# Optimization experiments

Measured on AMD Instinct MI355X. Metric: run time of the kernel, lower is better.

The kernel has to match this reference:

```python
import jax, jax.numpy as jnp
import numpy as np

FRACS = (0.25, 0.5, 0.25)  # per-expert top-fraction kept, from the original forward


def setup_inputs() -> dict:
    key = jax.random.key(0)
    ks = jax.random.split(key, 10)
    B, S, D, P, E, C = 1, 65536, 1024, 512, 3, 2
    s = 0.02
    return {
        "hidden_states": jax.random.normal(ks[0], (B, S, D), jnp.float32),
        "W_t1": jax.random.normal(ks[1], (D, P), jnp.float32) * s,   # TransMIL stand-in proj
        "W_cls1": jax.random.normal(ks[2], (P, C), jnp.float32) * s, # trans1 bag classifier
        "Wg0": jax.random.normal(ks[3], (P, 2), jnp.float32) * s,    # gate
        "Wg1": jax.random.normal(ks[4], (P, 2), jnp.float32) * s,    # gate1
        "Wg2": jax.random.normal(ks[5], (P, 2), jnp.float32) * s,    # gate2
        "W_clf": jax.random.normal(ks[6], (E, P, E), jnp.float32) * s,  # per-expert classifiers
        "W_a1": jax.random.normal(ks[7], (P, P), jnp.float32) * s,   # agg1 TransMIL stand-in proj
        "W_acls": jax.random.normal(ks[8], (P, C), jnp.float32) * s, # agg1 bag classifier
    }


def reference(hidden_states, W_t1, W_cls1, Wg0, Wg1, Wg2, W_clf, W_a1, W_acls):
    B, S, D = hidden_states.shape
    x = hidden_states.reshape(-1, D)               # (T, D) tokens
    T = x.shape[0]
    # trans1 (TransMIL stand-in): per-patch feature + mean-pool bag logits
    patches = jnp.tanh(x @ W_t1)                   # (T, P) patch_feature
    bag = patches.mean(0)
    Y_logits = (bag @ W_cls1)[None, :]             # (1, C)
    Y_prob = jax.nn.softmax(Y_logits, -1)
    Y_hat = jnp.argmax(Y_logits, -1)
    # three independent routers, softmax + top-1
    router_logits = patches @ Wg0                  # (T, 2)
    rw0 = jax.nn.softmax(router_logits.astype(jnp.float32), -1)
    w_top0 = rw0.max(-1)                           # top-1 routing weight (gate0) used as sort key for ALL experts
    sel0 = jnp.argmax(rw0, -1)
    sel1 = jnp.argmax(jax.nn.softmax((patches @ Wg1).astype(jnp.float32), -1), -1)
    sel2 = jnp.argmax(jax.nn.softmax((patches @ Wg2).astype(jnp.float32), -1), -1)
    masks = [sel0 == 1, sel1 == 1, sel2 == 1]      # expert_mask[e][1] token selection
    joint_losses = jnp.float32(0.0)
    sel_fs, nums_list = [], []
    for e in range(3):
        mask = masks[e]
        cnt = mask.sum().astype(jnp.int32)
        nums = jnp.floor(cnt.astype(jnp.float32) * FRACS[e]).astype(jnp.int32)
        nums = jnp.where(nums == 0, cnt, nums)     # 'if nums != 0 else all' branch
        key_ = jnp.where(mask, w_top0, -jnp.inf)
        order = jnp.argsort(-key_)                 # descending routing weight
        rank = jnp.zeros(T, jnp.int32).at[order].set(jnp.arange(T, dtype=jnp.int32))
        sel = mask & (rank < nums)                 # top-fraction tokens of this expert
        sel_f = sel.astype(patches.dtype)
        mean_feat = (patches * sel_f[:, None]).sum(0) / jnp.maximum(nums, 1).astype(patches.dtype)
        logits = mean_feat @ W_clf[e]              # (3,)
        if e < 2:                                  # CE loss only for experts 0,1
            joint_losses = joint_losses + (-jax.nn.log_softmax(logits)[e])
        sel_fs.append(sel_f)
        nums_list.append(nums)
    # agg1 (TransMIL stand-in) over concatenated represent_patchs == multiplicity-weighted mean
    feats2 = jnp.tanh(patches @ W_a1)              # (T, P)
    total_sel = sel_fs[0] + sel_fs[1] + sel_fs[2]
    total_n = (nums_list[0] + nums_list[1] + nums_list[2]).astype(patches.dtype)
    agg_bag = (feats2 * total_sel[:, None]).sum(0) / jnp.maximum(total_n, 1.0)
    e_Y_logits = (agg_bag @ W_acls)[None, :]
    e_Y_hat = jnp.argmax(e_Y_logits, -1)
    distribute = jnp.stack([jnp.asarray(T, jnp.int32), nums_list[0], nums_list[1], nums_list[2]])
    return (e_Y_logits, e_Y_hat, Y_logits, Y_prob, Y_hat, router_logits, joint_losses, distribute)
```

## Files before the change

### kernel.cpp

```cpp
#include <hip/hip_runtime.h>
#include <cstdint>
#include <cstddef>

#define T_TOK 65536
#define DDIM  1024
#define PDIM  512

typedef __attribute__((ext_vector_type(8))) short          shortx8;
typedef __attribute__((ext_vector_type(8))) unsigned short ushortx8;
typedef __attribute__((ext_vector_type(4))) float          floatx4;

__device__ __forceinline__ unsigned short f2bf_rn(float x){
  unsigned int u = __float_as_uint(x);
  unsigned int r = u + 0x7FFFu + ((u >> 16) & 1u);
  return (unsigned short)(r >> 16);
}
__device__ __forceinline__ float bf2f(unsigned short h){
  return __uint_as_float(((unsigned int)h) << 16);
}
__device__ __forceinline__ float ftanh(float x){
  float ez = __expf(2.f * x);
  return 1.f - 2.f / (ez + 1.f);
}

__global__ void prep(const float* __restrict__ Wt1, const float* __restrict__ Wa1,
                     unsigned short* __restrict__ W1th, unsigned short* __restrict__ W1tl,
                     unsigned short* __restrict__ Wath, unsigned short* __restrict__ Watl,
                     int* __restrict__ zbase)
{
  int gid = blockIdx.x * 256 + threadIdx.x;
  if (gid < 20544){ zbase[gid] = 0; return; }
  int i = gid - 20544;
  if (i < 524288){
    int p = i >> 10, k = i & 1023;
    float x = Wt1[(size_t)k * PDIM + p];
    unsigned short h = f2bf_rn(x);
    W1th[i] = h;
    W1tl[i] = f2bf_rn(x - bf2f(h));
    return;
  }
  i -= 524288;
  if (i < 262144){
    int n = i >> 9, k = i & 511;
    float x = Wa1[(size_t)k * PDIM + n];
    unsigned short h = f2bf_rn(x);
    Wath[i] = h;
    Watl[i] = f2bf_rn(x - bf2f(h));
  }
}

template<int MODE>
__global__ __launch_bounds__(256, 2)
void gemm_split(const float* __restrict__ A,
                const unsigned short* __restrict__ Bhg,
                const unsigned short* __restrict__ Blg,
                float* __restrict__ Cout,
                float* __restrict__ colacc,
                const int* __restrict__ cidx,
                const float* __restrict__ wgt,
                const int* __restrict__ params)
{
  constexpr int K = (MODE == 0) ? 1024 : 512;
  __shared__ unsigned short Ah[128][40];
  __shared__ unsigned short Al[128][40];
  __shared__ unsigned short Bh[128][40];
  __shared__ unsigned short Bl[128][40];
  __shared__ int   cidxl[128];
  __shared__ float wl[128];

  const int tid = threadIdx.x;
  const int m0 = blockIdx.y * 128;
  const int n0 = blockIdx.x * 128;

  if (MODE == 1){
    int count = params[21];
    if (m0 >= count) return;
    if (tid < 128){
      int g = m0 + tid;
      if (g < count){ cidxl[tid] = cidx[g]; wl[tid] = wgt[g]; }
      else          { cidxl[tid] = 0;       wl[tid] = 0.f;   }
    }
    __syncthreads();
  }

  const int lane = tid & 63;
  const int wv   = tid >> 6;
  const int wm   = (wv & 1) << 6;
  const int wn   = (wv >> 1) << 6;
  const int lr   = lane & 15;
  const int quad = lane >> 4;
  const int kb8  = quad << 3;

  floatx4 acc[4][4];
  #pragma unroll
  for (int i = 0; i < 4; i++)
    #pragma unroll
    for (int j = 0; j < 4; j++)
      acc[i][j] = (floatx4){0.f, 0.f, 0.f, 0.f};

  const int nkb = K >> 5;
  for (int kb = 0; kb < nkb; ++kb){
    const int k0 = kb << 5;
    #pragma unroll
    for (int i = 0; i < 4; i++){
      int lin = i * 256 + tid;
      int row = lin >> 3;
      int kq  = (lin & 7) << 2;
      size_t arow = (MODE == 0) ? (size_t)(m0 + row) : (size_t)cidxl[row];
      const float4 v = *(const float4*)(A + arow * K + k0 + kq);
      unsigned int ux = __float_as_uint(v.x), uy = __float_as_uint(v.y);
      unsigned int uz = __float_as_uint(v.z), uw = __float_as_uint(v.w);
      float rx = v.x - __uint_as_float(ux & 0xFFFF0000u);
      float ry = v.y - __uint_as_float(uy & 0xFFFF0000u);
      float rz = v.z - __uint_as_float(uz & 0xFFFF0000u);
      float rw = v.w - __uint_as_float(uw & 0xFFFF0000u);
      ushort4 h, l;
      h.x = (unsigned short)(ux >> 16); l.x = (unsigned short)(__float_as_uint(rx) >> 16);
      h.y = (unsigned short)(uy >> 16); l.y = (unsigned short)(__float_as_uint(ry) >> 16);
      h.z = (unsigned short)(uz >> 16); l.z = (unsigned short)(__float_as_uint(rz) >> 16);
      h.w = (unsigned short)(uw >> 16); l.w = (unsigned short)(__float_as_uint(rw) >> 16);
      *(ushort4*)&Ah[row][kq] = h;
      *(ushort4*)&Al[row][kq] = l;
    }
    #pragma unroll
    for (int i = 0; i < 2; i++){
      int lin = i * 256 + tid;
      int row = lin >> 2;
      int kq  = (lin & 3) << 3;
      size_t off = (size_t)(n0 + row) * K + k0 + kq;
      *(ushortx8*)&Bh[row][kq] = *(const ushortx8*)(Bhg + off);
      *(ushortx8*)&Bl[row][kq] = *(const ushortx8*)(Blg + off);
    }
    __syncthreads();
    shortx8 a0[4], a1[4], b0[4], b1[4];
    #pragma unroll
    for (int i = 0; i < 4; i++){
      a0[i] = *(const shortx8*)&Ah[wm + i * 16 + lr][kb8];
      a1[i] = *(const shortx8*)&Al[wm + i * 16 + lr][kb8];
      b0[i] = *(const shortx8*)&Bh[wn + i * 16 + lr][kb8];
      b1[i] = *(const shortx8*)&Bl[wn + i * 16 + lr][kb8];
    }
    #pragma unroll
    for (int i = 0; i < 4; i++){
      #pragma unroll
      for (int j = 0; j < 4; j++){
        acc[i][j] = __builtin_amdgcn_mfma_f32_16x16x32_bf16(a0[i], b0[j], acc[i][j], 0, 0, 0);
        acc[i][j] = __builtin_amdgcn_mfma_f32_16x16x32_bf16(a1[i], b0[j], acc[i][j], 0, 0, 0);
        acc[i][j] = __builtin_amdgcn_mfma_f32_16x16x32_bf16(a0[i], b1[j], acc[i][j], 0, 0, 0);
      }
    }
    __syncthreads();
  }

  float csum[4] = {0.f, 0.f, 0.f, 0.f};
  #pragma unroll
  for (int i = 0; i < 4; i++){
    float w0 = 1.f, w1 = 1.f, w2 = 1.f, w3 = 1.f;
    if (MODE == 1){
      const float4 wv4 = *(const float4*)&wl[wm + i * 16 + (quad << 2)];
      w0 = wv4.x; w1 = wv4.y; w2 = wv4.z; w3 = wv4.w;
    }
    #pragma unroll
    for (int j = 0; j < 4; j++){
      float t0 = ftanh(acc[i][j][0]);
      float t1 = ftanh(acc[i][j][1]);
      float t2 = ftanh(acc[i][j][2]);
      float t3 = ftanh(acc[i][j][3]);
      if (MODE == 0){
        size_t base = (size_t)(m0 + wm + i * 16 + (quad << 2)) * PDIM + (n0 + wn + j * 16 + lr);
        Cout[base]            = t0;
        Cout[base +     PDIM] = t1;
        Cout[base + 2 * PDIM] = t2;
        Cout[base + 3 * PDIM] = t3;
        csum[j] += t0 + t1 + t2 + t3;
      } else {
        csum[j] += t0 * w0 + t1 * w1 + t2 * w2 + t3 * w3;
      }
    }
  }
  #pragma unroll
  for (int j = 0; j < 4; j++){
    float s = csum[j];
    s += __shfl_xor(s, 16);
    s += __shfl_xor(s, 32);
    if (lane < 16) atomicAdd(&colacc[n0 + wn + j * 16 + lane], s);
  }
}

__global__ void gates_kernel(const float* __restrict__ patches,
                             const float* __restrict__ Wg0,
                             const float* __restrict__ Wg1,
                             const float* __restrict__ Wg2,
                             float* __restrict__ dout,
                             unsigned int* __restrict__ wkey,
                             unsigned char* __restrict__ mask3,
                             int* __restrict__ params,
                             int* __restrict__ hist)
{
  __shared__ int lc[3];
  const int tid = threadIdx.x;
  if (tid < 3) lc[tid] = 0;
  __syncthreads();
  const int lane = tid & 63;
  float wg[3][16];
  const float* Wgp[3] = {Wg0, Wg1, Wg2};
  #pragma unroll
  for (int g = 0; g < 3; g++){
    #pragma unroll
    for (int j = 0; j < 4; j++){
      float4 v = *(const float4*)(Wgp[g] + lane * 16 + j * 4);
      wg[g][j * 4 + 0] = v.x; wg[g][j * 4 + 1] = v.y;
      wg[g][j * 4 + 2] = v.z; wg[g][j * 4 + 3] = v.w;
    }
  }
  const int nw = gridDim.x << 2;
  for (int t = blockIdx.x * 4 + (tid >> 6); t < T_TOK; t += nw){
    const float* row = patches + (size_t)t * PDIM + lane * 8;
    float4 v0 = *(const float4*)row;
    float4 v1 = *(const float4*)(row + 4);
    float x[8] = {v0.x, v0.y, v0.z, v0.w, v1.x, v1.y, v1.z, v1.w};
    float g00 = 0, g01 = 0, g10 = 0, g11 = 0, g20 = 0, g21 = 0;
    #pragma unroll
    for (int j = 0; j < 8; j++){
      g00 += x[j] * wg[0][2 * j]; g01 += x[j] * wg[0][2 * j + 1];
      g10 += x[j] * wg[1][2 * j]; g11 += x[j] * wg[1][2 * j + 1];
      g20 += x[j] * wg[2][2 * j]; g21 += x[j] * wg[2][2 * j + 1];
    }
    #pragma unroll
    for (int off = 1; off < 64; off <<= 1){
      g00 += __shfl_xor(g00, off); g01 += __shfl_xor(g01, off);
      g10 += __shfl_xor(g10, off); g11 += __shfl_xor(g11, off);
      g20 += __shfl_xor(g20, off); g21 += __shfl_xor(g21, off);
    }
    if (lane == 0){
      dout[8 + 2 * t]     = g00;
      dout[8 + 2 * t + 1] = g01;
      int m0 = g01 > g00;
      int m1 = g11 > g10;
      int m2 = g21 > g20;
      mask3[t] = (unsigned char)(m0 | (m1 << 1) | (m2 << 2));
      float d = fabsf(g00 - g01);
      float w = 1.0f / (1.0f + __expf(-d));
      unsigned int u = __float_as_uint(w);
      u = u < 0x3F000000u ? 0x3F000000u : u;
      u = u > 0x3F7FFFFFu ? 0x3F7FFFFFu : u;
      wkey[t] = u;
      int b = (int)((u >> 11) & 0xFFFu);
      if (m0){ atomicAdd(&hist[b], 1);         atomicAdd(&lc[0], 1); }
      if (m1){ atomicAdd(&hist[4096 + b], 1);  atomicAdd(&lc[1], 1); }
      if (m2){ atomicAdd(&hist[8192 + b], 1);  atomicAdd(&lc[2], 1); }
    }
  }
  __syncthreads();
  if (tid < 3 && lc[tid]) atomicAdd(&params[tid], lc[tid]);
}

__global__ void find_bucket(int* __restrict__ params, const int* __restrict__ hist)
{
  __shared__ int cs[256], orig[256];
  __shared__ int selc, selrk;
  const int tid = threadIdx.x;
  for (int e = 0; e < 3; e++){
    int cnt = params[e];
    int shift = (e == 1) ? 1 : 2;
    int nums = cnt >> shift;
    if (nums == 0) nums = cnt;
    if (tid == 0) params[3 + e] = nums;
    __syncthreads();
    if (nums == 0){
      if (tid == 0){ params[6 + e] = -1; params[9 + e] = 0; }
      __syncthreads();
      continue;
    }
    const int* h = hist + e * 4096 + tid * 16;
    int s = 0;
    #pragma unroll
    for (int j = 0; j < 16; j++) s += h[j];
    cs[tid] = s; orig[tid] = s;
    __syncthreads();
    for (int off = 1; off < 256; off <<= 1){
      int v = (tid + off < 256) ? cs[tid + off] : 0;
      __syncthreads();
      cs[tid] += v;
      __syncthreads();
    }
    if (cs[tid] >= nums && (cs[tid] - orig[tid]) < nums){
      selc = tid; selrk = nums - (cs[tid] - orig[tid]);
    }
    __syncthreads();
    if (tid == 0){
      int ch = selc, rk = selrk;
      const int* hh = hist + e * 4096 + ch * 16;
      int acc = 0;
      for (int j = 15; j >= 0; j--){
        int c = hh[j];
        if (acc + c >= rk){ params[6 + e] = ch * 16 + j; params[9 + e] = rk - acc; break; }
        acc += c;
      }
    }
    __syncthreads();
  }
}

__global__ void level2hist(const int* __restrict__ params, const unsigned int* __restrict__ wkey,
                           const unsigned char* __restrict__ mask3, int* __restrict__ h2)
{
  const int e = blockIdx.y;
  const int B = params[6 + e];
  if (B < 0) return;
  const unsigned char bit = (unsigned char)(1u << e);
  const int t0 = blockIdx.x * 2048 + threadIdx.x;
  #pragma unroll
  for (int i = 0; i < 8; i++){
    int t = t0 + i * 256;
    if (mask3[t] & bit){
      unsigned int u = wkey[t];
      if ((int)((u >> 11) & 0xFFFu) == B) atomicAdd(&h2[e * 2048 + (u & 2047u)], 1);
    }
  }
}

__global__ void find_theta(int* __restrict__ params, const int* __restrict__ h2)
{
  const int e = blockIdx.x;
  const int tid = threadIdx.x;
  __shared__ int cs[256], orig[256];
  __shared__ int selc;
  int B = params[6 + e], rank = params[9 + e];
  if (B < 0){
    if (tid == 0){ params[12 + e] = (int)0xFFFFFFFFu; params[15 + e] = 0; params[18 + e] = 0; }
    return;
  }
  const int* h = h2 + e * 2048 + tid * 8;
  int s = 0;
  #pragma unroll
  for (int j = 0; j < 8; j++) s += h[j];
  cs[tid] = s; orig[tid] = s;
  __syncthreads();
  for (int off = 1; off < 256; off <<= 1){
    int v = (tid + off < 256) ? cs[tid + off] : 0;
    __syncthreads();
    cs[tid] += v;
    __syncthreads();
  }
  if (cs[tid] >= rank && (cs[tid] - orig[tid]) < rank) selc = tid;
  __syncthreads();
  if (tid == 0){
    int ch = selc;
    int rk = rank - (cs[ch] - orig[ch]);
    const int* hh = h2 + e * 2048 + ch * 8;
    int acc = 0;
    for (int j = 7; j >= 0; j--){
      int c = hh[j];
      if (acc + c >= rk){
        int sub = ch * 8 + j;
        params[12 + e] = (int)(0x3F000000u | ((unsigned)B << 11) | (unsigned)sub);
        params[15 + e] = rk - acc;
        params[18 + e] = c;
        break;
      }
      acc += c;
    }
  }
}

__global__ void mark_sel(const int* __restrict__ params, const unsigned int* __restrict__ wkey,
                         const unsigned char* __restrict__ mask3, unsigned char* __restrict__ selb)
{
  const int e = blockIdx.y;
  const int bx = blockIdx.x;
  const int tid = threadIdx.x;
  const unsigned int theta = (unsigned int)params[12 + e];
  const int r = params[15 + e];
  const int ceq = params[18 + e];
  const unsigned char bit = (unsigned char)(1u << e);
  unsigned char* sb = selb + e * T_TOK;
  if (ceq == r){
    int t0 = bx * 2048;
    #pragma unroll
    for (int i = 0; i < 8; i++){
      int t = t0 + i * 256 + tid;
      unsigned char mk = mask3[t] & bit;
      sb[t] = (mk && wkey[t] >= theta) ? 1 : 0;
    }
  } else {
    if (bx) return;
    __shared__ int basec;
    __shared__ int wsum[4];
    if (tid == 0) basec = 0;
    __syncthreads();
    const int lane = tid & 63, w = tid >> 6;
    for (int c = 0; c < 256; c++){
      int t = c * 256 + tid;
      unsigned char mk = mask3[t] & bit;
      unsigned int u = mk ? wkey[t] : 0u;
      bool gt = mk && (u > theta);
      bool eq = mk && (u == theta);
      unsigned long long bal = __ballot(eq);
      if (lane == 0) wsum[w] = __popcll(bal);
      __syncthreads();
      int wbase = 0;
      for (int ww = 0; ww < w; ww++) wbase += wsum[ww];
      int pos = basec + wbase + __popcll(bal & ((1ull << lane) - 1ull));
      sb[t] = (gt || (eq && pos < r)) ? 1 : 0;
      __syncthreads();
      if (tid == 0) basec += wsum[0] + wsum[1] + wsum[2] + wsum[3];
      __syncthreads();
    }
  }
}

__global__ void compact(const unsigned char* __restrict__ selb, int* __restrict__ cidx,
                        float* __restrict__ wgt, int* __restrict__ params)
{
  int t = blockIdx.x * 256 + threadIdx.x;
  int ts = selb[t] + selb[T_TOK + t] + selb[2 * T_TOK + t];
  int lane = threadIdx.x & 63;
  unsigned long long bal = __ballot(ts > 0);
  int base = 0;
  if (lane == 0) base = atomicAdd(&params[21], __popcll(bal));
  base = __shfl(base, 0);
  if (ts){
    int pos = base + __popcll(bal & ((1ull << lane) - 1ull));
    cidx[pos] = t;
    wgt[pos] = (float)ts;
  }
}

__global__ void meanfeat_c(const float* __restrict__ patches, const unsigned char* __restrict__ selb,
                           const int* __restrict__ cidx, const int* __restrict__ params,
                           float* __restrict__ mf)
{
  const int count = params[21];
  const int base = blockIdx.x * 256;
  if (base >= count) return;
  const int n = min(256, count - base);
  const int tid = threadIdx.x;
  __shared__ int cl[256];
  __shared__ unsigned char f0s[256], f1s[256];
  if (tid < n){
    int c = cidx[base + tid];
    cl[tid] = c;
    f0s[tid] = selb[c];
    f1s[tid] = selb[T_TOK + c];
  }
  __syncthreads();
  float s00 = 0, s01 = 0, s10 = 0, s11 = 0;
  for (int i = 0; i < n; i++){
    int f0 = f0s[i], f1 = f1s[i];
    if (f0 | f1){
      float2 v = *(const float2*)(patches + (size_t)cl[i] * PDIM + tid * 2);
      if (f0){ s00 += v.x; s01 += v.y; }
      if (f1){ s10 += v.x; s11 += v.y; }
    }
  }
  atomicAdd(&mf[tid * 2],       s00);
  atomicAdd(&mf[tid * 2 + 1],   s01);
  atomicAdd(&mf[512 + tid * 2],     s10);
  atomicAdd(&mf[512 + tid * 2 + 1], s11);
}

__global__ void finalize(const float* __restrict__ bagsum, const float* __restrict__ aggsum,
                         const float* __restrict__ mf, const int* __restrict__ params,
                         const float* __restrict__ Wcls1, const float* __restrict__ Wclf,
                         const float* __restrict__ Wacls, float* __restrict__ dout)
{
  const int lane = threadIdx.x;
  const int nums0 = params[3], nums1 = params[4], nums2 = params[5];
  const float invT = 1.0f / 65536.0f;
  const float inv0 = 1.0f / (float)(nums0 > 0 ? nums0 : 1);
  const float inv1 = 1.0f / (float)(nums1 > 0 ? nums1 : 1);
  const float totn = (float)(nums0 + nums1 + nums2);
  const float invA = 1.0f / fmaxf(totn, 1.0f);
  float y0 = 0, y1 = 0, a0 = 0, a1 = 0;
  float l00 = 0, l01 = 0, l02 = 0, l10 = 0, l11 = 0, l12 = 0;
  #pragma unroll
  for (int j = 0; j < 8; j++){
    int p = lane * 8 + j;
    float bg = bagsum[p] * invT;
    y0 += bg * Wcls1[p * 2]; y1 += bg * Wcls1[p * 2 + 1];
    float ag = aggsum[p] * invA;
    a0 += ag * Wacls[p * 2]; a1 += ag * Wacls[p * 2 + 1];
    float m0v = mf[p] * inv0;
    l00 += m0v * Wclf[p * 3]; l01 += m0v * Wclf[p * 3 + 1]; l02 += m0v * Wclf[p * 3 + 2];
    float m1v = mf[512 + p] * inv1;
    l10 += m1v * Wclf[1536 + p * 3]; l11 += m1v * Wclf[1536 + p * 3 + 1]; l12 += m1v * Wclf[1536 + p * 3 + 2];
  }
  #pragma unroll
  for (int off = 1; off < 64; off <<= 1){
    y0 += __shfl_xor(y0, off);   y1 += __shfl_xor(y1, off);
    a0 += __shfl_xor(a0, off);   a1 += __shfl_xor(a1, off);
    l00 += __shfl_xor(l00, off); l01 += __shfl_xor(l01, off); l02 += __shfl_xor(l02, off);
    l10 += __shfl_xor(l10, off); l11 += __shfl_xor(l11, off); l12 += __shfl_xor(l12, off);
  }
  if (lane == 0){
    dout[0] = a0; dout[1] = a1;
    dout[2] = (a1 > a0) ? 1.0f : 0.0f;
    dout[3] = y0; dout[4] = y1;
    float mx = fmaxf(y0, y1), e0 = expf(y0 - mx), e1 = expf(y1 - mx), inv = 1.0f / (e0 + e1);
    dout[5] = e0 * inv; dout[6] = e1 * inv;
    dout[7] = (y1 > y0) ? 1.0f : 0.0f;
    float m3 = fmaxf(fmaxf(l00, l01), l02);
    float lse0 = m3 + logf(expf(l00 - m3) + expf(l01 - m3) + expf(l02 - m3));
    float m4 = fmaxf(fmaxf(l10, l11), l12);
    float lse1 = m4 + logf(expf(l10 - m4) + expf(l11 - m4) + expf(l12 - m4));
    dout[131080] = (lse0 - l00) + (lse1 - l11);
    dout[131081] = 65536.0f;
    dout[131082] = (float)nums0;
    dout[131083] = (float)nums1;
    dout[131084] = (float)nums2;
  }
}

extern "C" void kernel_launch(void* const* d_in, const int* in_sizes, int n_in,
                              void* d_out, int out_size, void* d_ws, size_t ws_size,
                              hipStream_t stream)
{
  const float* X      = (const float*)d_in[0];
  const float* W_t1   = (const float*)d_in[1];
  const float* W_cls1 = (const float*)d_in[2];
  const float* Wg0    = (const float*)d_in[3];
  const float* Wg1    = (const float*)d_in[4];
  const float* Wg2    = (const float*)d_in[5];
  const float* W_clf  = (const float*)d_in[6];
  const float* W_a1   = (const float*)d_in[7];
  const float* W_acls = (const float*)d_in[8];
  float* dout = (float*)d_out;
  char* ws = (char*)d_ws;

  float*          patches = (float*)         (ws + 0);
  unsigned short* W1th    = (unsigned short*)(ws + 134217728);
  unsigned short* W1tl    = (unsigned short*)(ws + 135266304);
  unsigned short* Wath    = (unsigned short*)(ws + 136314880);
  unsigned short* Watl    = (unsigned short*)(ws + 136839168);
  unsigned int*   wkey    = (unsigned int*)  (ws + 137363456);
  unsigned char*  mask3   = (unsigned char*) (ws + 137625600);
  unsigned char*  selb    = (unsigned char*) (ws + 137691136);
  int*            cidx    = (int*)           (ws + 137887744);
  float*          wgt     = (float*)         (ws + 138149888);
  int*            zbase   = (int*)           (ws + 138412032);
  int*            hist    = zbase;
  int*            h2      = zbase + 12288;
  int*            params  = zbase + 18432;
  float*          bagsum  = (float*)(zbase + 18496);
  float*          aggsum  = (float*)(zbase + 19008);
  float*          mf      = (float*)(zbase + 19520);

  prep<<<3153, 256, 0, stream>>>(W_t1, W_a1, W1th, W1tl, Wath, Watl, zbase);

  gemm_split<0><<<dim3(4, 512), 256, 0, stream>>>(
      X, W1th, W1tl, patches, bagsum, nullptr, nullptr, nullptr);

  gates_kernel<<<512, 256, 0, stream>>>(
      patches, Wg0, Wg1, Wg2, dout, wkey, mask3, params, hist);

  find_bucket<<<1, 256, 0, stream>>>(params, hist);
  level2hist<<<dim3(32, 3), 256, 0, stream>>>(params, wkey, mask3, h2);
  find_theta<<<3, 256, 0, stream>>>(params, h2);
  mark_sel<<<dim3(32, 3), 256, 0, stream>>>(params, wkey, mask3, selb);
  compact<<<256, 256, 0, stream>>>(selb, cidx, wgt, params);

  meanfeat_c<<<256, 256, 0, stream>>>(patches, selb, cidx, params, mf);

  gemm_split<1><<<dim3(4, 512), 256, 0, stream>>>(
      patches, Wath, Watl, nullptr, aggsum, cidx, wgt, params);

  finalize<<<1, 64, 0, stream>>>(bagsum, aggsum, mf, params, W_cls1, W_clf, W_acls, dout);
}
```

Baseline: 716.8 us.

## Fuse gate logits into main GEMM, store patches as bf16, swizzle LDS

The router-gate dot products now run in the epilogue of the first GEMM. Partial logits are reduced with shuffles and atomically added into a per-token buffer, so the separate pass that re-read the full fp32 patches matrix is gone. Patches are stored as bf16, which halves that write and the later reads. The second GEMM drops the split-precision low parts and runs a single bf16 MFMA. LDS tiles use an XOR swizzle instead of padding, and occupancy rises to 4 blocks per SM; the cost is lower precision in the router logits and the downstream aggregation, plus many more atomics.

```diff
diff --git a/kernel.cpp b/kernel.cpp
--- a/kernel.cpp
+++ b/kernel.cpp
@@ -22,15 +22,28 @@
   float ez = __expf(2.f * x);
   return 1.f - 2.f / (ez + 1.f);
 }
+__device__ __forceinline__ int lds_off(int row, int q){
+  return row * 32 + ((q ^ ((row >> 1) & 3)) << 3);
+}
+__device__ __forceinline__ void split8(const float4& a, const float4& b,
+                                       ushortx8& h, ushortx8& l){
+  float x[8] = {a.x, a.y, a.z, a.w, b.x, b.y, b.z, b.w};
+  #pragma unroll
+  for (int i = 0; i < 8; i++){
+    unsigned int u = __float_as_uint(x[i]);
+    float r = x[i] - __uint_as_float(u & 0xFFFF0000u);
+    h[i] = (unsigned short)(u >> 16);
+    l[i] = (unsigned short)(__float_as_uint(r) >> 16);
+  }
+}
 
 __global__ void prep(const float* __restrict__ Wt1, const float* __restrict__ Wa1,
                      unsigned short* __restrict__ W1th, unsigned short* __restrict__ W1tl,
-                     unsigned short* __restrict__ Wath, unsigned short* __restrict__ Watl,
-                     int* __restrict__ zbase)
+                     unsigned short* __restrict__ Wath, int* __restrict__ zbase)
 {
   int gid = blockIdx.x * 256 + threadIdx.x;
-  if (gid < 20544){ zbase[gid] = 0; return; }
-  int i = gid - 20544;
+  if (gid < 413760){ zbase[gid] = 0; return; }
+  int i = gid - 413760;
   if (i < 524288){
     int p = i >> 10, k = i & 1023;
     float x = Wt1[(size_t)k * PDIM + p];
@@ -42,46 +55,29 @@
   i -= 524288;
   if (i < 262144){
     int n = i >> 9, k = i & 511;
-    float x = Wa1[(size_t)k * PDIM + n];
-    unsigned short h = f2bf_rn(x);
-    Wath[i] = h;
-    Watl[i] = f2bf_rn(x - bf2f(h));
-  }
-}
-
-template<int MODE>
-__global__ __launch_bounds__(256, 2)
-void gemm_split(const float* __restrict__ A,
-                const unsigned short* __restrict__ Bhg,
-                const unsigned short* __restrict__ Blg,
-                float* __restrict__ Cout,
-                float* __restrict__ colacc,
-                const int* __restrict__ cidx,
-                const float* __restrict__ wgt,
-                const int* __restrict__ params)
-{
-  constexpr int K = (MODE == 0) ? 1024 : 512;
-  __shared__ unsigned short Ah[128][40];
-  __shared__ unsigned short Al[128][40];
-  __shared__ unsigned short Bh[128][40];
-  __shared__ unsigned short Bl[128][40];
-  __shared__ int   cidxl[128];
-  __shared__ float wl[128];
+    Wath[i] = f2bf_rn(Wa1[(size_t)k * PDIM + n]);
+  }
+}
+
+__global__ __launch_bounds__(256, 4)
+void gemm_main(const float* __restrict__ A,
+               const unsigned short* __restrict__ Bhg,
+               const unsigned short* __restrict__ Blg,
+               unsigned short* __restrict__ Ptch,
+               float* __restrict__ bagsum,
+               float* __restrict__ glog,
+               const float* __restrict__ Wg0,
+               const float* __restrict__ Wg1,
+               const float* __restrict__ Wg2)
+{
+  __shared__ __align__(16) unsigned short Ah[4096];
+  __shared__ __align__(16) unsigned short Al[4096];
+  __shared__ __align__(16) unsigned short Bh[4096];
+  __shared__ __align__(16) unsigned short Bl[4096];
 
   const int tid = threadIdx.x;
   const int m0 = blockIdx.y * 128;
   const int n0 = blockIdx.x * 128;
-
-  if (MODE == 1){
-    int count = params[21];
-    if (m0 >= count) return;
-    if (tid < 128){
-      int g = m0 + tid;
-      if (g < count){ cidxl[tid] = cidx[g]; wl[tid] = wgt[g]; }
-      else          { cidxl[tid] = 0;       wl[tid] = 0.f;   }
-    }
-    __syncthreads();
-  }
 
   const int lane = tid & 63;
   const int wv   = tid >> 6;
@@ -89,7 +85,11 @@
   const int wn   = (wv >> 1) << 6;
   const int lr   = lane & 15;
   const int quad = lane >> 4;
-  const int kb8  = quad << 3;
+
+  const int arow = tid >> 1;
+  const int akh  = (tid & 1) << 4;
+  const int aq0  = (tid & 1) << 1;
+  const float* asrc = A + (size_t)(m0 + arow) * DDIM + akh;
 
   floatx4 acc[4][4];
   #pragma unroll
@@ -98,47 +98,41 @@
     for (int j = 0; j < 4; j++)
       acc[i][j] = (floatx4){0.f, 0.f, 0.f, 0.f};
 
-  const int nkb = K >> 5;
-  for (int kb = 0; kb < nkb; ++kb){
+  for (int kb = 0; kb < 32; ++kb){
     const int k0 = kb << 5;
+    {
+      float4 v0 = *(const float4*)(asrc + k0);
+      float4 v1 = *(const float4*)(asrc + k0 + 4);
+      float4 v2 = *(const float4*)(asrc + k0 + 8);
+      float4 v3 = *(const float4*)(asrc + k0 + 12);
+      ushortx8 h0, l0, h1, l1;
+      split8(v0, v1, h0, l0);
+      split8(v2, v3, h1, l1);
+      *(ushortx8*)&Ah[lds_off(arow, aq0)]     = h0;
+      *(ushortx8*)&Ah[lds_off(arow, aq0 + 1)] = h1;
+      *(ushortx8*)&Al[lds_off(arow, aq0)]     = l0;
+      *(ushortx8*)&Al[lds_off(arow, aq0 + 1)] = l1;
+    }
+    #pragma unroll
+    for (int it = 0; it < 2; it++){
+      int lin = it * 256 + tid;
+      int row = lin >> 2;
+      int qb  = lin & 3;
+      size_t off = (size_t)(n0 + row) * DDIM + k0 + qb * 8;
+      ushortx8 bh = *(const ushortx8*)(Bhg + off);
+      ushortx8 bl = *(const ushortx8*)(Blg + off);
+      int d = lds_off(row, qb);
+      *(ushortx8*)&Bh[d] = bh;
+      *(ushortx8*)&Bl[d] = bl;
+    }
+    __syncthreads();
+    shortx8 a0[4], a1[4], b0[4], b1[4];
     #pragma unroll
     for (int i = 0; i < 4; i++){
-      int lin = i * 256 + tid;
-      int row = lin >> 3;
-      int kq  = (lin & 7) << 2;
-      size_t arow = (MODE == 0) ? (size_t)(m0 + row) : (size_t)cidxl[row];
-      const float4 v = *(const float4*)(A + arow * K + k0 + kq);
-      unsigned int ux = __float_as_uint(v.x), uy = __float_as_uint(v.y);
-      unsigned int uz = __float_as_uint(v.z), uw = __float_as_uint(v.w);
-      float rx = v.x - __uint_as_float(ux & 0xFFFF0000u);
-      float ry = v.y - __uint_as_float(uy & 0xFFFF0000u);
-      float rz = v.z - __uint_as_float(uz & 0xFFFF0000u);
-      float rw = v.w - __uint_as_float(uw & 0xFFFF0000u);
-      ushort4 h, l;
-      h.x = (unsigned short)(ux >> 16); l.x = (unsigned short)(__float_as_uint(rx) >> 16);
-      h.y = (unsigned short)(uy >> 16); l.y = (unsigned short)(__float_as_uint(ry) >> 16);
-      h.z = (unsigned short)(uz >> 16); l.z = (unsigned short)(__float_as_uint(rz) >> 16);
-      h.w = (unsigned short)(uw >> 16); l.w = (unsigned short)(__float_as_uint(rw) >> 16);
-      *(ushort4*)&Ah[row][kq] = h;
-      *(ushort4*)&Al[row][kq] = l;
-    }
-    #pragma unroll
-    for (int i = 0; i < 2; i++){
-      int lin = i * 256 + tid;
-      int row = lin >> 2;
-      int kq  = (lin & 3) << 3;
-      size_t off = (size_t)(n0 + row) * K + k0 + kq;
-      *(ushortx8*)&Bh[row][kq] = *(const ushortx8*)(Bhg + off);
-      *(ushortx8*)&Bl[row][kq] = *(const ushortx8*)(Blg + off);
-    }
-    __syncthreads();
-    shortx8 a0[4], a1[4], b0[4], b1[4];
-    #pragma unroll
-    for (int i = 0; i < 4; i++){
-      a0[i] = *(const shortx8*)&Ah[wm + i * 16 + lr][kb8];
-      a1[i] = *(const shortx8*)&Al[wm + i * 16 + lr][kb8];
-      b0[i] = *(const shortx8*)&Bh[wn + i * 16 + lr][kb8];
-      b1[i] = *(const shortx8*)&Bl[wn + i * 16 + lr][kb8];
+      a0[i] = *(const shortx8*)&Ah[lds_off(wm + i * 16 + lr, quad)];
+      a1[i] = *(const shortx8*)&Al[lds_off(wm + i * 16 + lr, quad)];
+      b0[i] = *(const shortx8*)&Bh[lds_off(wn + i * 16 + lr, quad)];
+      b1[i] = *(const shortx8*)&Bl[lds_off(wn + i * 16 + lr, quad)];
     }
     #pragma unroll
     for (int i = 0; i < 4; i++){
@@ -152,30 +146,58 @@
     __syncthreads();
   }
 
+  float wgr[4][6];
+  #pragma unroll
+  for (int j = 0; j < 4; j++){
+    int c = n0 + wn + j * 16 + lr;
+    wgr[j][0] = Wg0[c * 2]; wgr[j][1] = Wg0[c * 2 + 1];
+    wgr[j][2] = Wg1[c * 2]; wgr[j][3] = Wg1[c * 2 + 1];
+    wgr[j][4] = Wg2[c * 2]; wgr[j][5] = Wg2[c * 2 + 1];
+  }
+
   float csum[4] = {0.f, 0.f, 0.f, 0.f};
   #pragma unroll
   for (int i = 0; i < 4; i++){
-    float w0 = 1.f, w1 = 1.f, w2 = 1.f, w3 = 1.f;
-    if (MODE == 1){
-      const float4 wv4 = *(const float4*)&wl[wm + i * 16 + (quad << 2)];
-      w0 = wv4.x; w1 = wv4.y; w2 = wv4.z; w3 = wv4.w;
-    }
+    float gp[4][6];
+    #pragma unroll
+    for (int k = 0; k < 4; k++)
+      #pragma unroll
+      for (int g = 0; g < 6; g++) gp[k][g] = 0.f;
+    const int row = m0 + wm + i * 16 + quad * 4;
     #pragma unroll
     for (int j = 0; j < 4; j++){
       float t0 = ftanh(acc[i][j][0]);
       float t1 = ftanh(acc[i][j][1]);
       float t2 = ftanh(acc[i][j][2]);
       float t3 = ftanh(acc[i][j][3]);
-      if (MODE == 0){
-        size_t base = (size_t)(m0 + wm + i * 16 + (quad << 2)) * PDIM + (n0 + wn + j * 16 + lr);
-        Cout[base]            = t0;
-        Cout[base +     PDIM] = t1;
-        Cout[base + 2 * PDIM] = t2;
-        Cout[base + 3 * PDIM] = t3;
-        csum[j] += t0 + t1 + t2 + t3;
-      } else {
-        csum[j] += t0 * w0 + t1 * w1 + t2 * w2 + t3 * w3;
+      const int col = n0 + wn + j * 16 + lr;
+      Ptch[(size_t)(row + 0) * PDIM + col] = f2bf_rn(t0);
+      Ptch[(size_t)(row + 1) * PDIM + col] = f2bf_rn(t1);
+      Ptch[(size_t)(row + 2) * PDIM + col] = f2bf_rn(t2);
+      Ptch[(size_t)(row + 3) * PDIM + col] = f2bf_rn(t3);
+      csum[j] += t0 + t1 + t2 + t3;
+      #pragma unroll
+      for (int g = 0; g < 6; g++){
+        gp[0][g] += t0 * wgr[j][g];
+        gp[1][g] += t1 * wgr[j][g];
+        gp[2][g] += t2 * wgr[j][g];
+        gp[3][g] += t3 * wgr[j][g];
       }
+    }
+    #pragma unroll
+    for (int s = 1; s < 16; s <<= 1){
+      #pragma unroll
+      for (int k = 0; k < 4; k++)
+        #pragma unroll
+        for (int g = 0; g < 6; g++)
+          gp[k][g] += __shfl_xor(gp[k][g], s);
+    }
+    if (lr == 0){
+      #pragma unroll
+      for (int k = 0; k < 4; k++)
+        #pragma unroll
+        for (int g = 0; g < 6; g++)
+          atomicAdd(&glog[(size_t)(row + k) * 6 + g], gp[k][g]);
     }
   }
   #pragma unroll
@@ -183,74 +205,38 @@
     float s = csum[j];
     s += __shfl_xor(s, 16);
     s += __shfl_xor(s, 32);
-    if (lane < 16) atomicAdd(&colacc[n0 + wn + j * 16 + lane], s);
-  }
-}
-
-__global__ void gates_kernel(const float* __restrict__ patches,
-                             const float* __restrict__ Wg0,
-                             const float* __restrict__ Wg1,
-                             const float* __restrict__ Wg2,
-                             float* __restrict__ dout,
-                             unsigned int* __restrict__ wkey,
-                             unsigned char* __restrict__ mask3,
-                             int* __restrict__ params,
-                             int* __restrict__ hist)
+    if (lane < 16) atomicAdd(&bagsum[n0 + wn + j * 16 + lane], s);
+  }
+}
+
+__global__ void gates_small(const float* __restrict__ glog, float* __restrict__ dout,
+                            unsigned int* __restrict__ wkey, unsigned char* __restrict__ mask3,
+                            int* __restrict__ params, int* __restrict__ hist)
 {
   __shared__ int lc[3];
   const int tid = threadIdx.x;
   if (tid < 3) lc[tid] = 0;
   __syncthreads();
-  const int lane = tid & 63;
-  float wg[3][16];
-  const float* Wgp[3] = {Wg0, Wg1, Wg2};
-  #pragma unroll
-  for (int g = 0; g < 3; g++){
-    #pragma unroll
-    for (int j = 0; j < 4; j++){
-      float4 v = *(const float4*)(Wgp[g] + lane * 16 + j * 4);
-      wg[g][j * 4 + 0] = v.x; wg[g][j * 4 + 1] = v.y;
-      wg[g][j * 4 + 2] = v.z; wg[g][j * 4 + 3] = v.w;
-    }
-  }
-  const int nw = gridDim.x << 2;
-  for (int t = blockIdx.x * 4 + (tid >> 6); t < T_TOK; t += nw){
-    const float* row = patches + (size_t)t * PDIM + lane * 8;
-    float4 v0 = *(const float4*)row;
-    float4 v1 = *(const float4*)(row + 4);
-    float x[8] = {v0.x, v0.y, v0.z, v0.w, v1.x, v1.y, v1.z, v1.w};
-    float g00 = 0, g01 = 0, g10 = 0, g11 = 0, g20 = 0, g21 = 0;
-    #pragma unroll
-    for (int j = 0; j < 8; j++){
-      g00 += x[j] * wg[0][2 * j]; g01 += x[j] * wg[0][2 * j + 1];
-      g10 += x[j] * wg[1][2 * j]; g11 += x[j] * wg[1][2 * j + 1];
-      g20 += x[j] * wg[2][2 * j]; g21 += x[j] * wg[2][2 * j + 1];
-    }
-    #pragma unroll
-    for (int off = 1; off < 64; off <<= 1){
-      g00 += __shfl_xor(g00, off); g01 += __shfl_xor(g01, off);
-      g10 += __shfl_xor(g10, off); g11 += __shfl_xor(g11, off);
-      g20 += __shfl_xor(g20, off); g21 += __shfl_xor(g21, off);
-    }
-    if (lane == 0){
-      dout[8 + 2 * t]     = g00;
-      dout[8 + 2 * t + 1] = g01;
-      int m0 = g01 > g00;
-      int m1 = g11 > g10;
-      int m2 = g21 > g20;
-      mask3[t] = (unsigned char)(m0 | (m1 << 1) | (m2 << 2));
-      float d = fabsf(g00 - g01);
-      float w = 1.0f / (1.0f + __expf(-d));
-      unsigned int u = __float_as_uint(w);
-      u = u < 0x3F000000u ? 0x3F000000u : u;
-      u = u > 0x3F7FFFFFu ? 0x3F7FFFFFu : u;
-      wkey[t] = u;
-      int b = (int)((u >> 11) & 0xFFFu);
-      if (m0){ atomicAdd(&hist[b], 1);         atomicAdd(&lc[0], 1); }
-      if (m1){ atomicAdd(&hist[4096 + b], 1);  atomicAdd(&lc[1], 1); }
-      if (m2){ atomicAdd(&hist[8192 + b], 1);  atomicAdd(&lc[2], 1); }
-    }
-  }
+  const int t = blockIdx.x * 256 + tid;
+  float2 p0 = *(const float2*)(glog + (size_t)t * 6);
+  float2 p1 = *(const float2*)(glog + (size_t)t * 6 + 2);
+  float2 p2 = *(const float2*)(glog + (size_t)t * 6 + 4);
+  dout[8 + 2 * t]     = p0.x;
+  dout[8 + 2 * t + 1] = p0.y;
+  int m0 = p0.y > p0.x;
+  int m1 = p1.y > p1.x;
+  int m2 = p2.y > p2.x;
+  mask3[t] = (unsigned char)(m0 | (m1 << 1) | (m2 << 2));
+  float d = fabsf(p0.x - p0.y);
+  float w = 1.0f / (1.0f + __expf(-d));
+  unsigned int u = __float_as_uint(w);
+  u = u < 0x3F000000u ? 0x3F000000u : u;
+  u = u > 0x3F7FFFFFu ? 0x3F7FFFFFu : u;
+  wkey[t] = u;
+  int b = (int)((u >> 11) & 0xFFFu);
+  if (m0){ atomicAdd(&hist[b], 1);        atomicAdd(&lc[0], 1); }
+  if (m1){ atomicAdd(&hist[4096 + b], 1); atomicAdd(&lc[1], 1); }
+  if (m2){ atomicAdd(&hist[8192 + b], 1); atomicAdd(&lc[2], 1); }
   __syncthreads();
   if (tid < 3 && lc[tid]) atomicAdd(&params[tid], lc[tid]);
 }
@@ -427,7 +413,8 @@
   }
 }
 
-__global__ void meanfeat_c(const float* __restrict__ patches, const unsigned char* __restrict__ selb,
+__global__ void meanfeat_c(const unsigned short* __restrict__ Ptch,
+                           const unsigned char* __restrict__ selb,
                            const int* __restrict__ cidx, const int* __restrict__ params,
                            float* __restrict__ mf)
 {
@@ -449,15 +436,111 @@
   for (int i = 0; i < n; i++){
     int f0 = f0s[i], f1 = f1s[i];
     if (f0 | f1){
-      float2 v = *(const float2*)(patches + (size_t)cl[i] * PDIM + tid * 2);
-      if (f0){ s00 += v.x; s01 += v.y; }
-      if (f1){ s10 += v.x; s11 += v.y; }
-    }
-  }
-  atomicAdd(&mf[tid * 2],       s00);
-  atomicAdd(&mf[tid * 2 + 1],   s01);
+      unsigned int u = *(const unsigned int*)(Ptch + (size_t)cl[i] * PDIM + tid * 2);
+      float vx = bf2f((unsigned short)(u & 0xFFFFu));
+      float vy = bf2f((unsigned short)(u >> 16));
+      if (f0){ s00 += vx; s01 += vy; }
+      if (f1){ s10 += vx; s11 += vy; }
+    }
+  }
+  atomicAdd(&mf[tid * 2],           s00);
+  atomicAdd(&mf[tid * 2 + 1],       s01);
   atomicAdd(&mf[512 + tid * 2],     s10);
   atomicAdd(&mf[512 + tid * 2 + 1], s11);
+}
+
+__global__ __launch_bounds__(256, 4)
+void gemm_agg(const unsigned short* __restrict__ Ptch,
+              const unsigned short* __restrict__ Bhg,
+              float* __restrict__ aggsum,
+              const int* __restrict__ cidx,
+              const float* __restrict__ wgt,
+              const int* __restrict__ params)
+{
+  __shared__ __align__(16) unsigned short Ah[4096];
+  __shared__ __align__(16) unsigned short Bh[4096];
+  __shared__ int   cidxl[128];
+  __shared__ float wl[128];
+
+  const int tid = threadIdx.x;
+  const int m0 = blockIdx.y * 128;
+  const int n0 = blockIdx.x * 128;
+  const int count = params[21];
+  if (m0 >= count) return;
+  if (tid < 128){
+    int g = m0 + tid;
+    if (g < count){ cidxl[tid] = cidx[g]; wl[tid] = wgt[g]; }
+    else          { cidxl[tid] = 0;       wl[tid] = 0.f;   }
+  }
+  __syncthreads();
+
+  const int lane = tid & 63;
+  const int wv   = tid >> 6;
+  const int wm   = (wv & 1) << 6;
+  const int wn   = (wv >> 1) << 6;
+  const int lr   = lane & 15;
+  const int quad = lane >> 4;
+
+  const int arow = tid >> 1;
+  const int akh  = (tid & 1) << 4;
+  const int aq0  = (tid & 1) << 1;
+  const unsigned short* asrc = Ptch + (size_t)cidxl[arow] * PDIM + akh;
+
+  floatx4 acc[4][4];
+  #pragma unroll
+  for (int i = 0; i < 4; i++)
+    #pragma unroll
+    for (int j = 0; j < 4; j++)
+      acc[i][j] = (floatx4){0.f, 0.f, 0.f, 0.f};
+
+  for (int kb = 0; kb < 16; ++kb){
+    const int k0 = kb << 5;
+    {
+      ushortx8 h0 = *(const ushortx8*)(asrc + k0);
+      ushortx8 h1 = *(const ushortx8*)(asrc + k0 + 8);
+      *(ushortx8*)&Ah[lds_off(arow, aq0)]     = h0;
+      *(ushortx8*)&Ah[lds_off(arow, aq0 + 1)] = h1;
+    }
+    #pragma unroll
+    for (int it = 0; it < 2; it++){
+      int lin = it * 256 + tid;
+      int row = lin >> 2;
+      int qb  = lin & 3;
+      ushortx8 bh = *(const ushortx8*)(Bhg + (size_t)(n0 + row) * PDIM + k0 + qb * 8);
+      *(ushortx8*)&Bh[lds_off(row, qb)] = bh;
+    }
+    __syncthreads();
+    shortx8 a0[4], b0[4];
+    #pragma unroll
+    for (int i = 0; i < 4; i++){
+      a0[i] = *(const shortx8*)&Ah[lds_off(wm + i * 16 + lr, quad)];
+      b0[i] = *(const shortx8*)&Bh[lds_off(wn + i * 16 + lr, quad)];
+    }
+    #pragma unroll
+    for (int i = 0; i < 4; i++)
+      #pragma unroll
+      for (int j = 0; j < 4; j++)
+        acc[i][j] = __builtin_amdgcn_mfma_f32_16x16x32_bf16(a0[i], b0[j], acc[i][j], 0, 0, 0);
+    __syncthreads();
+  }
+
+  float csum[4] = {0.f, 0.f, 0.f, 0.f};
+  #pragma unroll
+  for (int i = 0; i < 4; i++){
+    const float4 wv4 = *(const float4*)&wl[wm + i * 16 + (quad << 2)];
+    #pragma unroll
+    for (int j = 0; j < 4; j++){
+      csum[j] += ftanh(acc[i][j][0]) * wv4.x + ftanh(acc[i][j][1]) * wv4.y
+               + ftanh(acc[i][j][2]) * wv4.z + ftanh(acc[i][j][3]) * wv4.w;
+    }
+  }
+  #pragma unroll
+  for (int j = 0; j < 4; j++){
+    float s = csum[j];
+    s += __shfl_xor(s, 16);
+    s += __shfl_xor(s, 32);
+    if (lane < 16) atomicAdd(&aggsum[n0 + wn + j * 16 + lane], s);
+  }
 }
 
 __global__ void finalize(const float* __restrict__ bagsum, const float* __restrict__ aggsum,
@@ -528,31 +611,30 @@
   float* dout = (float*)d_out;
   char* ws = (char*)d_ws;
 
-  float*          patches = (float*)         (ws + 0);
-  unsigned short* W1th    = (unsigned short*)(ws + 134217728);
-  unsigned short* W1tl    = (unsigned short*)(ws + 135266304);
-  unsigned short* Wath    = (unsigned short*)(ws + 136314880);
-  unsigned short* Watl    = (unsigned short*)(ws + 136839168);
-  unsigned int*   wkey    = (unsigned int*)  (ws + 137363456);
-  unsigned char*  mask3   = (unsigned char*) (ws + 137625600);
-  unsigned char*  selb    = (unsigned char*) (ws + 137691136);
-  int*            cidx    = (int*)           (ws + 137887744);
-  float*          wgt     = (float*)         (ws + 138149888);
-  int*            zbase   = (int*)           (ws + 138412032);
-  int*            hist    = zbase;
-  int*            h2      = zbase + 12288;
-  int*            params  = zbase + 18432;
-  float*          bagsum  = (float*)(zbase + 18496);
-  float*          aggsum  = (float*)(zbase + 19008);
-  float*          mf      = (float*)(zbase + 19520);
-
-  prep<<<3153, 256, 0, stream>>>(W_t1, W_a1, W1th, W1tl, Wath, Watl, zbase);
-
-  gemm_split<0><<<dim3(4, 512), 256, 0, stream>>>(
-      X, W1th, W1tl, patches, bagsum, nullptr, nullptr, nullptr);
-
-  gates_kernel<<<512, 256, 0, stream>>>(
-      patches, Wg0, Wg1, Wg2, dout, wkey, mask3, params, hist);
+  unsigned short* Ptch  = (unsigned short*)(ws + 0);
+  unsigned short* W1th  = (unsigned short*)(ws + 67108864);
+  unsigned short* W1tl  = (unsigned short*)(ws + 68157440);
+  unsigned short* Wath  = (unsigned short*)(ws + 69206016);
+  unsigned int*   wkey  = (unsigned int*)  (ws + 69730304);
+  unsigned char*  mask3 = (unsigned char*) (ws + 69992448);
+  unsigned char*  selb  = (unsigned char*) (ws + 70057984);
+  int*            cidx  = (int*)           (ws + 70254592);
+  float*          wgt   = (float*)         (ws + 70516736);
+  int*            zbase = (int*)           (ws + 70778880);
+  float* glog   = (float*)zbase;
+  int*   hist   = zbase + 393216;
+  int*   h2     = zbase + 405504;
+  int*   params = zbase + 411648;
+  float* bagsum = (float*)(zbase + 411712);
+  float* aggsum = (float*)(zbase + 412224);
+  float* mf     = (float*)(zbase + 412736);
+
+  prep<<<4689, 256, 0, stream>>>(W_t1, W_a1, W1th, W1tl, Wath, zbase);
+
+  gemm_main<<<dim3(4, 512), 256, 0, stream>>>(
+      X, W1th, W1tl, Ptch, bagsum, glog, Wg0, Wg1, Wg2);
+
+  gates_small<<<256, 256, 0, stream>>>(glog, dout, wkey, mask3, params, hist);
 
   find_bucket<<<1, 256, 0, stream>>>(params, hist);
   level2hist<<<dim3(32, 3), 256, 0, stream>>>(params, wkey, mask3, h2);
@@ -560,10 +642,9 @@
   mark_sel<<<dim3(32, 3), 256, 0, stream>>>(params, wkey, mask3, selb);
   compact<<<256, 256, 0, stream>>>(selb, cidx, wgt, params);
 
-  meanfeat_c<<<256, 256, 0, stream>>>(patches, selb, cidx, params, mf);
-
-  gemm_split<1><<<dim3(4, 512), 256, 0, stream>>>(
-      patches, Wath, Watl, nullptr, aggsum, cidx, wgt, params);
+  meanfeat_c<<<256, 256, 0, stream>>>(Ptch, selb, cidx, params, mf);
+
+  gemm_agg<<<dim3(4, 512), 256, 0, stream>>>(Ptch, Wath, aggsum, cidx, wgt, params);
 
   finalize<<<1, 64, 0, stream>>>(bagsum, aggsum, mf, params, W_cls1, W_clf, W_acls, dout);
 }
```

New measurement: 923.8 us. 28.9% more time.
